# Kernel optimization log

Hardware: AMD Instinct MI355X
Metric: run time of the kernel (lower is better)

Reference implementation:

```python
import jax, jax.numpy as jnp
import numpy as np

B, T, D, H = 2, 2048, 1024, 16
NEG = -65504.0


def setup_inputs() -> dict:
    key = jax.random.key(0)
    ks = jax.random.split(key, 12)
    std = float(np.sqrt(2.0 / (D + D)))  # xavier_normal for square weights
    inp = {
        'q': jax.random.normal(ks[0], (B, T, D), jnp.float32),
        'k': jax.random.normal(ks[1], (B, T, D), jnp.float32),
        'v': jax.random.normal(ks[2], (B, T, D), jnp.float32),
        'mask': jax.random.randint(ks[3], (B, T), 0, 2, jnp.int32),
        # weights stored as (in, out) so y = x @ W + b
        'Wq': jax.random.normal(ks[4], (D, D), jnp.float32) * std,
        'bq': jnp.zeros((D,), jnp.float32),
        'Wk': jax.random.normal(ks[5], (D, D), jnp.float32) * std,
        'bk': jnp.zeros((D,), jnp.float32),
        'Wv': jax.random.normal(ks[6], (D, D), jnp.float32) * std,
        'bv': jnp.zeros((D,), jnp.float32),
        'Wo': jax.random.normal(ks[7], (D, D), jnp.float32) * std,
        'bo': jnp.zeros((D,), jnp.float32),
    }
    return inp


def reference(q, k, v, mask, Wq, bq, Wk, bk, Wv, bv, Wo, bo):
    b, t, _ = q.shape
    dim_a = Wq.shape[1]
    dh = dim_a // H
    # projections, then split into heads: (b, t, H, dh)
    qh = (q @ Wq + bq).reshape(b, t, H, dh)
    kh = (k @ Wk + bk).reshape(b, t, H, dh)
    vh = (v @ Wv + bv).reshape(b, t, H, dh)
    # NOTE: module scales by 1/sqrt(dim_a) with the FULL dim_a, not per-head
    a = jnp.einsum('bthd,bshd->bhts', qh, kh) / jnp.sqrt(jnp.float32(dim_a))
    # 2D mask broadcasts over query positions: (b, 1, 1, t_keys)
    a = jnp.where(mask[:, None, None, :] == 0, NEG, a)
    a = jax.nn.softmax(a, axis=-1)  # dropout_prob=0 (eval mode)
    o = jnp.einsum('bhts,bshd->bthd', a, vh).reshape(b, t, dim_a)
    return o @ Wo + bo
```

## Files before the change

kernel.cpp:

```cpp
#include <hip/hip_runtime.h>
#include <hip/hip_bf16.h>
#include <math.h>

#define B_ 2
#define T_ 2048
#define D_ 1024
#define H_ 16
#define QSCALE (0.03125f * 1.44269504088896f)

typedef _Float16 f16;
using f16x4 = __attribute__((ext_vector_type(4))) _Float16;
using f16x8 = __attribute__((ext_vector_type(8))) _Float16;
using f32x4 = __attribute__((ext_vector_type(4))) float;

__device__ __forceinline__ void gl16(const void* g, void* l) {
  __builtin_amdgcn_global_load_lds(
      (__attribute__((address_space(1))) void*)g,
      (__attribute__((address_space(3))) void*)l, 16, 0, 0);
}

__global__ __launch_bounds__(256) void prep(
    const float* __restrict__ q, const float* __restrict__ k,
    const float* __restrict__ v, const int* __restrict__ mask,
    const float* __restrict__ Wq, const float* __restrict__ Wk,
    const float* __restrict__ Wv, const float* __restrict__ Wo,
    const float* __restrict__ bq, const float* __restrict__ bk,
    const float* __restrict__ bv, const float* __restrict__ bo,
    f16* __restrict__ xqkv, f16* __restrict__ Wt, float* __restrict__ bias,
    int* __restrict__ idx, int* __restrict__ inv, int* __restrict__ nk,
    f16* __restrict__ khc) {
  __shared__ float sh[64][65];
  const int bid = blockIdx.x;
  const int tid = threadIdx.x;

  if (bid < 6144) {
    const int z = bid / 2048;
    const float* src = (z == 0) ? q : (z == 1) ? k : v;
    const size_t i = ((size_t)(bid % 2048) * 256 + tid) * 8;
    float4 a = *(const float4*)(src + i);
    float4 b = *(const float4*)(src + i + 4);
    f16x8 o;
    o[0] = (f16)a.x; o[1] = (f16)a.y; o[2] = (f16)a.z; o[3] = (f16)a.w;
    o[4] = (f16)b.x; o[5] = (f16)b.y; o[6] = (f16)b.z; o[7] = (f16)b.w;
    *(f16x8*)(xqkv + (size_t)z * 4194304 + i) = o;
  } else if (bid < 7168) {
    const int id = bid - 6144;
    const int z = id >> 8;
    const int k0 = ((id >> 4) & 15) * 64, n0 = (id & 15) * 64;
    const float* W = (z == 0) ? Wq : (z == 1) ? Wk : (z == 2) ? Wv : Wo;
    const int r = tid >> 2, c0 = (tid & 3) * 16;
#pragma unroll
    for (int i = 0; i < 4; ++i)
      *(float4*)&sh[r][c0 + 4 * i] =
          *(const float4*)&W[(size_t)(k0 + r) * 1024 + n0 + c0 + 4 * i];
    __syncthreads();
    f16 tmp[16];
#pragma unroll
    for (int i = 0; i < 16; ++i) tmp[i] = (f16)sh[c0 + i][r];
    f16* dst = Wt + (size_t)z * 1048576 + (size_t)(n0 + r) * 1024 + k0 + c0;
    *(f16x8*)dst = *(f16x8*)&tmp[0];
    *(f16x8*)(dst + 8) = *(f16x8*)&tmp[8];
  } else if (bid < 7184) {
    const int i = (bid - 7168) * 256 + tid;
    const int z = i >> 10;
    const float* s = (z == 0) ? bq : (z == 1) ? bk : (z == 2) ? bv : bo;
    bias[i] = s[i & 1023];
  } else {
    const int b = bid - 7184;
    int* cnt = (int*)sh;
    int loc[8];
    int c = 0;
#pragma unroll
    for (int i = 0; i < 8; ++i) {
      loc[i] = mask[b * T_ + tid * 8 + i];
      c += loc[i];
    }
    cnt[tid] = c;
    __syncthreads();
    for (int off = 1; off < 256; off <<= 1) {
      int vsh = (tid >= off) ? cnt[tid - off] : 0;
      __syncthreads();
      cnt[tid] += vsh;
      __syncthreads();
    }
    int pos = cnt[tid] - c;
#pragma unroll
    for (int i = 0; i < 8; ++i) {
      const int t = tid * 8 + i;
      if (loc[i]) {
        idx[b * T_ + pos] = t;
        inv[b * T_ + t] = pos;
        ++pos;
      } else {
        inv[b * T_ + t] = -1;
      }
    }
    const int n = cnt[255];
    if (tid == 255) nk[b] = n;
    const int nkt = (n + 63) >> 6;
    const int npadrows = (nkt << 6) - n;
    uint4 z4 = {0u, 0u, 0u, 0u};
    f16* base = khc + ((size_t)b * T_ + n) * D_;
    for (int i = tid; i < npadrows * 128; i += 256)
      *(uint4*)(base + (size_t)i * 8) = z4;
  }
}

__global__ __launch_bounds__(256) void gemm_qkv(
    const f16* __restrict__ Xb, const f16* __restrict__ Wtb,
    const float* __restrict__ biasb, f16* __restrict__ qh,
    f16* __restrict__ khc, f16* __restrict__ vh,
    const int* __restrict__ inv) {
  __shared__ __align__(16) f16 As[128 * 32];
  __shared__ __align__(16) f16 Bs[128 * 32];
  const int z = blockIdx.z;
  const f16* X = Xb + (size_t)z * 4194304;
  const f16* Wt = Wtb + (size_t)z * 1048576;
  const float* bias = biasb + (size_t)z * 1024;
  f16* C = (z == 0) ? qh : (z == 1) ? khc : vh;

  const int tid = threadIdx.x;
  const int wave = tid >> 6, lane = tid & 63;
  const int quad = lane >> 4, l16 = lane & 15;
  const int wm = wave & 1, wn = wave >> 1;
  const int m0 = blockIdx.y * 128, n0 = blockIdx.x * 128;

  f32x4 acc[4][4] = {};

  const f16* asrc = X + (size_t)(m0 + (tid >> 2)) * 1024 + (tid & 3) * 8;
  const f16* bsrc = Wt + (size_t)(n0 + (tid >> 2)) * 1024 + (tid & 3) * 8;
  char* aldst = (char*)As + tid * 16;
  char* bldst = (char*)Bs + tid * 16;

  for (int kt = 0; kt < 32; ++kt) {
    if (kt) __syncthreads();
    gl16(asrc, aldst);
    gl16(asrc + 65536, aldst + 4096);
    gl16(bsrc, bldst);
    gl16(bsrc + 65536, bldst + 4096);
    asrc += 32; bsrc += 32;
    __syncthreads();

    f16x8 af[4], bf[4];
#pragma unroll
    for (int t = 0; t < 4; ++t)
      af[t] = *(const f16x8*)&As[(64 * wm + 16 * t + l16) * 32 + quad * 8];
#pragma unroll
    for (int t = 0; t < 4; ++t)
      bf[t] = *(const f16x8*)&Bs[(64 * wn + 16 * t + l16) * 32 + quad * 8];
#pragma unroll
    for (int i = 0; i < 4; ++i)
#pragma unroll
      for (int j = 0; j < 4; ++j)
        acc[i][j] = __builtin_amdgcn_mfma_f32_16x16x32_f16(af[i], bf[j], acc[i][j], 0, 0, 0);
  }

  const int cm = m0 + 64 * wm + 4 * quad;
  const int cn = n0 + 64 * wn + l16;
  float bv[4];
#pragma unroll
  for (int tn = 0; tn < 4; ++tn) bv[tn] = bias[cn + 16 * tn];

  if (z == 1) {
    const int bb = m0 >> 11;
#pragma unroll
    for (int tm = 0; tm < 4; ++tm) {
#pragma unroll
      for (int r = 0; r < 4; ++r) {
        const int m = cm + 16 * tm + r;
        const int j = inv[m];
        if (j >= 0) {
          f16* row = C + ((size_t)(bb << 11) + j) * 1024;
#pragma unroll
          for (int tn = 0; tn < 4; ++tn)
            row[cn + 16 * tn] = (f16)(acc[tm][tn][r] + bv[tn]);
        }
      }
    }
  } else {
    const float scl = (z == 0) ? QSCALE : 1.f;
#pragma unroll
    for (int tm = 0; tm < 4; ++tm)
#pragma unroll
      for (int r = 0; r < 4; ++r) {
        f16* row = C + (size_t)(cm + 16 * tm + r) * 1024;
#pragma unroll
        for (int tn = 0; tn < 4; ++tn)
          row[cn + 16 * tn] = (f16)((acc[tm][tn][r] + bv[tn]) * scl);
      }
  }
}

__global__ __launch_bounds__(256) void vtrans(
    const f16* __restrict__ vh, const int* __restrict__ idx,
    const int* __restrict__ nk, f16* __restrict__ vhT) {
  const int tt = blockIdx.x, bh = blockIdx.y;
  const int b = bh >> 4, h = bh & 15;
  const int n = nk[b];
  const int nkt = (n + 63) >> 6;
  if (tt >= nkt) return;
  __shared__ f16 t[64][72];
  const int tid = threadIdx.x;
  const int r = tid >> 2, cq = 16 * (tid & 3);

  const int j = tt * 64 + r;
  uint4 v0 = {0u, 0u, 0u, 0u}, v1 = {0u, 0u, 0u, 0u};
  if (j < n) {
    const int tsrc = idx[b * T_ + j];
    const uint4* src = (const uint4*)(vh + ((size_t)b * T_ + tsrc) * D_ + h * 64 + cq);
    v0 = src[0]; v1 = src[1];
  }
  *(uint4*)&t[r][cq]     = v0;
  *(uint4*)&t[r][cq + 8] = v1;
  __syncthreads();

  f16 tmp[16];
#pragma unroll
  for (int xx = 0; xx < 16; ++xx) {
    int x = (xx + r) & 15;
    tmp[x] = t[cq + x][r];
  }
  f16* dst = vhT + ((size_t)bh * 64 + r) * T_ + tt * 64 + cq;
  *(uint4*)&dst[0] = *(uint4*)&tmp[0];
  *(uint4*)&dst[8] = *(uint4*)&tmp[8];
}

__global__ __launch_bounds__(256) void attn_mfma(
    const f16* __restrict__ qh, const f16* __restrict__ khc,
    const f16* __restrict__ vhT, const int* __restrict__ nkd,
    f16* __restrict__ opart, float* __restrict__ lpart) {
  __shared__ f16 Ks[64][72];
  __shared__ f16 Vt[64][72];
  __shared__ f16 Ps[4][32][72];

  const int qt = blockIdx.x, bh = blockIdx.y, ks = blockIdx.z;
  const int b = bh >> 4, h = bh & 15;
  const int tid = threadIdx.x;
  const int wave = tid >> 6, lane = tid & 63;
  const int quad = lane >> 4, l16 = lane & 15;
  const int sr = tid >> 2, sq = 16 * (tid & 3);

  const int n = nkd[b];
  const int nkt = (n + 63) >> 6;
  const int hn = (nkt + 1) >> 1;
  const int t_begin = ks ? hn : 0;
  const int t_end = ks ? nkt : hn;
  const bool owns_last = (t_end == nkt) && (t_end > t_begin);
  const int npad = (nkt << 6) - n;

  f16x8 qf[2][2];
#pragma unroll
  for (int gq = 0; gq < 2; ++gq) {
    const f16* qp = qh + ((size_t)(b * T_ + qt * 128 + wave * 32 + 16 * gq + l16)) * D_ + h * 64 + quad * 8;
    qf[gq][0] = *(const f16x8*)qp;
    qf[gq][1] = *(const f16x8*)(qp + 32);
  }

  float lsum[2] = {0.f, 0.f};
  f32x4 o[2][4] = {};

  const f16* kbase = khc + (size_t)b * T_ * D_ + h * 64;
  const f16* vbase = vhT + ((size_t)bh * 64 + sr) * T_;

  uint4 kr0, kr1, vr0, vr1;
  auto load_kv = [&](int kt) {
    const uint4* kp = (const uint4*)(kbase + (size_t)(kt * 64 + sr) * D_ + sq);
    kr0 = kp[0]; kr1 = kp[1];
    const uint4* vp = (const uint4*)(vbase + kt * 64 + sq);
    vr0 = vp[0]; vr1 = vp[1];
  };
  if (t_begin < t_end) load_kv(t_begin);

  for (int kt = t_begin; kt < t_end; ++kt) {
    *(uint4*)&Ks[sr][sq]     = kr0;
    *(uint4*)&Ks[sr][sq + 8] = kr1;
    *(uint4*)&Vt[sr][sq]     = vr0;
    *(uint4*)&Vt[sr][sq + 8] = vr1;
    __syncthreads();
    if (kt + 1 < t_end) load_kv(kt + 1);

#pragma unroll
    for (int tn = 0; tn < 4; ++tn) {
      f16x8 kf0 = *(const f16x8*)&Ks[16 * tn + l16][quad * 8];
      f16x8 kf1 = *(const f16x8*)&Ks[16 * tn + l16][32 + quad * 8];
#pragma unroll
      for (int gq = 0; gq < 2; ++gq) {
        f32x4 s = {0.f, 0.f, 0.f, 0.f};
        s = __builtin_amdgcn_mfma_f32_16x16x32_f16(kf0, qf[gq][0], s, 0, 0, 0);
        s = __builtin_amdgcn_mfma_f32_16x16x32_f16(kf1, qf[gq][1], s, 0, 0, 0);
        float p0 = exp2f(s[0]), p1 = exp2f(s[1]);
        float p2 = exp2f(s[2]), p3 = exp2f(s[3]);
        lsum[gq] += (p0 + p1) + (p2 + p3);
        f16x4 pk;
        pk[0] = (f16)p0; pk[1] = (f16)p1; pk[2] = (f16)p2; pk[3] = (f16)p3;
        *(f16x4*)&Ps[wave][16 * gq + l16][16 * tn + 4 * quad] = pk;
      }
    }

    f16x8 pf[2][2];
#pragma unroll
    for (int gq = 0; gq < 2; ++gq) {
      pf[gq][0] = *(const f16x8*)&Ps[wave][16 * gq + l16][quad * 8];
      pf[gq][1] = *(const f16x8*)&Ps[wave][16 * gq + l16][32 + quad * 8];
    }
#pragma unroll
    for (int t = 0; t < 4; ++t) {
      f16x8 vf0 = *(const f16x8*)&Vt[16 * t + l16][quad * 8];
      f16x8 vf1 = *(const f16x8*)&Vt[16 * t + l16][32 + quad * 8];
#pragma unroll
      for (int gq = 0; gq < 2; ++gq) {
        o[gq][t] = __builtin_amdgcn_mfma_f32_16x16x32_f16(pf[gq][0], vf0, o[gq][t], 0, 0, 0);
        o[gq][t] = __builtin_amdgcn_mfma_f32_16x16x32_f16(pf[gq][1], vf1, o[gq][t], 0, 0, 0);
      }
    }
    __syncthreads();
  }

  f16* obase = opart + (size_t)ks * 4194304;
  float* lbase = lpart + (size_t)ks * 65536 + (size_t)bh * 2048;
#pragma unroll
  for (int gq = 0; gq < 2; ++gq) {
    float ls = lsum[gq];
    ls += __shfl_xor(ls, 16);
    ls += __shfl_xor(ls, 32);
    if (owns_last) ls -= (float)npad;
    const int qrow0 = qt * 128 + wave * 32 + 16 * gq;
    if (quad == 0) lbase[qrow0 + l16] = ls;
    const size_t orow = (size_t)(b * T_ + qrow0 + 4 * quad);
#pragma unroll
    for (int r = 0; r < 4; ++r)
#pragma unroll
      for (int t = 0; t < 4; ++t)
        obase[(orow + r) * D_ + h * 64 + 16 * t + l16] = (f16)o[gq][t][r];
  }
}

__global__ __launch_bounds__(256) void gemm_out(
    const f16* __restrict__ opart, const float* __restrict__ lpart,
    const f16* __restrict__ Wt3, const float* __restrict__ bias3,
    float* __restrict__ out) {
  __shared__ __align__(16) f16 As[64 * 32];
  __shared__ __align__(16) f16 Bs[128 * 32];
  const int tid = threadIdx.x;
  const int wave = tid >> 6, lane = tid & 63;
  const int quad = lane >> 4, l16 = lane & 15;
  const int wm = wave & 1, wn = wave >> 1;
  const int m0 = blockIdx.y * 64, n0 = blockIdx.x * 128;

  f32x4 acc[2][4] = {};

  const int row = m0 + (tid >> 2);
  const int cq = (tid & 3) * 8;
  const f16* oa = opart + (size_t)row * 1024 + cq;
  const f16* ob = oa + 4194304;
  const float* lp = lpart + (size_t)(row >> 11) * 32768 + (row & 2047);
  const f16* bsrc = Wt3 + (size_t)(n0 + (tid >> 2)) * 1024 + cq;
  char* bldst = (char*)Bs + tid * 16;

  for (int kt = 0; kt < 32; ++kt) {
    if (kt) __syncthreads();
    gl16(bsrc, bldst);
    gl16(bsrc + 65536, bldst + 4096);
    bsrc += 32;
    const int h = (kt * 32 + cq) >> 6;
    const float la = lp[h * 2048];
    const float lb = lp[65536 + h * 2048];
    const float invl = 1.f / (la + lb);
    f16x8 a8 = *(const f16x8*)(oa + kt * 32);
    f16x8 b8 = *(const f16x8*)(ob + kt * 32);
    f16x8 hv;
#pragma unroll
    for (int i = 0; i < 8; ++i)
      hv[i] = (f16)(((float)a8[i] + (float)b8[i]) * invl);
    *(f16x8*)(As + tid * 8) = hv;
    __syncthreads();

    f16x8 af[2], bf[4];
#pragma unroll
    for (int t = 0; t < 2; ++t)
      af[t] = *(const f16x8*)&As[(32 * wm + 16 * t + l16) * 32 + quad * 8];
#pragma unroll
    for (int t = 0; t < 4; ++t)
      bf[t] = *(const f16x8*)&Bs[(64 * wn + 16 * t + l16) * 32 + quad * 8];
#pragma unroll
    for (int i = 0; i < 2; ++i)
#pragma unroll
      for (int j = 0; j < 4; ++j)
        acc[i][j] = __builtin_amdgcn_mfma_f32_16x16x32_f16(af[i], bf[j], acc[i][j], 0, 0, 0);
  }

  const int cm = m0 + 32 * wm + 4 * quad;
  const int cn = n0 + 64 * wn + l16;
#pragma unroll
  for (int tn = 0; tn < 4; ++tn) {
    const float bv = bias3[cn + 16 * tn];
#pragma unroll
    for (int tm = 0; tm < 2; ++tm)
#pragma unroll
      for (int r = 0; r < 4; ++r)
        out[(size_t)(cm + 16 * tm + r) * 1024 + cn + 16 * tn] = acc[tm][tn][r] + bv;
  }
}

extern "C" void kernel_launch(void* const* d_in, const int* in_sizes, int n_in,
                              void* d_out, int out_size, void* d_ws, size_t ws_size,
                              hipStream_t stream) {
  const float* q  = (const float*)d_in[0];
  const float* k  = (const float*)d_in[1];
  const float* v  = (const float*)d_in[2];
  const int* mask = (const int*)d_in[3];
  const float* Wq = (const float*)d_in[4];
  const float* bq = (const float*)d_in[5];
  const float* Wk = (const float*)d_in[6];
  const float* bk = (const float*)d_in[7];
  const float* Wv = (const float*)d_in[8];
  const float* bv = (const float*)d_in[9];
  const float* Wo = (const float*)d_in[10];
  const float* bo = (const float*)d_in[11];
  float* out = (float*)d_out;

  char* ws = (char*)d_ws;
  f16* xqkv   = (f16*)(ws);
  f16* Wt     = (f16*)(ws + 25165824);
  f16* qh     = (f16*)(ws + 33554432);
  f16* vh     = (f16*)(ws + 41943040);
  f16* khc    = (f16*)(ws + 50331648);
  float* lpart = (float*)(ws + 58720256);
  float* bsw  = (float*)(ws + 59244544);
  int* idx    = (int*)(ws + 59260928);
  int* inv    = (int*)(ws + 59277312);
  int* nk     = (int*)(ws + 59293696);
  f16* vhT    = (f16*)(ws);
  f16* opart  = (f16*)(ws + 8388608);

  dim3 blk(256);

  prep<<<dim3(7186), blk, 0, stream>>>(q, k, v, mask, Wq, Wk, Wv, Wo,
                                       bq, bk, bv, bo, xqkv, Wt, bsw,
                                       idx, inv, nk, khc);

  gemm_qkv<<<dim3(8, 32, 3), blk, 0, stream>>>(xqkv, Wt, bsw,
                                               qh, khc, vh, inv);

  vtrans<<<dim3(32, 32), blk, 0, stream>>>(vh, idx, nk, vhT);

  attn_mfma<<<dim3(16, 32, 2), blk, 0, stream>>>(qh, khc, vhT, nk,
                                                 opart, lpart);

  gemm_out<<<dim3(8, 64), blk, 0, stream>>>(opart, lpart, Wt + 3145728,
                                            bsw + 3072, out);
}
```

Baseline: 230.4 us.

## Remap block IDs for XCD-local L2 reuse and prefetch A operand in out-proj

All three kernels (QKV GEMM, attention, output GEMM) now remap the linear block ID so that blocks sharing the same rows or heads land on the same XCD. The aim is better L2 reuse of shared A tiles and K/V data across the chiplets. In gemm_out, the 16 per-head reciprocal softmax normalisers are computed once up front. The next A-operand partial outputs are also loaded into registers one iteration early, so global latency overlaps the MFMA work. The trade-off is extra register pressure from the invl array and the prefetched vectors.

```diff
diff --git a/kernel.cpp b/kernel.cpp
--- a/kernel.cpp
+++ b/kernel.cpp
@@ -113,7 +113,14 @@
     const int* __restrict__ inv) {
   __shared__ __align__(16) f16 As[128 * 32];
   __shared__ __align__(16) f16 Bs[128 * 32];
-  const int z = blockIdx.z;
+
+  const int bid = blockIdx.x + 8 * blockIdx.y + 256 * blockIdx.z;
+  const int xcd = bid & 7, local = bid >> 3;
+  const int gid = xcd * 12 + (local >> 3);
+  const int z = gid >> 5;
+  const int m0 = (gid & 31) * 128;
+  const int n0 = (local & 7) * 128;
+
   const f16* X = Xb + (size_t)z * 4194304;
   const f16* Wt = Wtb + (size_t)z * 1048576;
   const float* bias = biasb + (size_t)z * 1024;
@@ -123,7 +130,6 @@
   const int wave = tid >> 6, lane = tid & 63;
   const int quad = lane >> 4, l16 = lane & 15;
   const int wm = wave & 1, wn = wave >> 1;
-  const int m0 = blockIdx.y * 128, n0 = blockIdx.x * 128;
 
   f32x4 acc[4][4] = {};
 
@@ -233,8 +239,13 @@
   __shared__ f16 Vt[64][72];
   __shared__ f16 Ps[4][32][72];
 
-  const int qt = blockIdx.x, bh = blockIdx.y, ks = blockIdx.z;
+  const int bid = blockIdx.x + 16 * blockIdx.y + 512 * blockIdx.z;
+  const int xcd = bid & 7, local = bid >> 3;
+  const int qt = local & 15;
+  const int gh = xcd * 8 + (local >> 4);
+  const int bh = gh & 31, ks = gh >> 5;
   const int b = bh >> 4, h = bh & 15;
+
   const int tid = threadIdx.x;
   const int wave = tid >> 6, lane = tid & 63;
   const int quad = lane >> 4, l16 = lane & 15;
@@ -345,7 +356,11 @@
   const int wave = tid >> 6, lane = tid & 63;
   const int quad = lane >> 4, l16 = lane & 15;
   const int wm = wave & 1, wn = wave >> 1;
-  const int m0 = blockIdx.y * 64, n0 = blockIdx.x * 128;
+
+  const int bid = blockIdx.x + 8 * blockIdx.y;
+  const int xcd = bid & 7, local = bid >> 3;
+  const int m0 = (xcd * 8 + (local >> 3)) * 64;
+  const int n0 = (local & 7) * 128;
 
   f32x4 acc[2][4] = {};
 
@@ -354,26 +369,34 @@
   const f16* oa = opart + (size_t)row * 1024 + cq;
   const f16* ob = oa + 4194304;
   const float* lp = lpart + (size_t)(row >> 11) * 32768 + (row & 2047);
+
+  float invl[16];
+#pragma unroll
+  for (int h = 0; h < 16; ++h)
+    invl[h] = 1.f / (lp[h * 2048] + lp[65536 + h * 2048]);
+
   const f16* bsrc = Wt3 + (size_t)(n0 + (tid >> 2)) * 1024 + cq;
   char* bldst = (char*)Bs + tid * 16;
+
+  f16x8 a8 = *(const f16x8*)oa;
+  f16x8 b8 = *(const f16x8*)ob;
 
   for (int kt = 0; kt < 32; ++kt) {
     if (kt) __syncthreads();
     gl16(bsrc, bldst);
     gl16(bsrc + 65536, bldst + 4096);
     bsrc += 32;
-    const int h = (kt * 32 + cq) >> 6;
-    const float la = lp[h * 2048];
-    const float lb = lp[65536 + h * 2048];
-    const float invl = 1.f / (la + lb);
-    f16x8 a8 = *(const f16x8*)(oa + kt * 32);
-    f16x8 b8 = *(const f16x8*)(ob + kt * 32);
+    const float iv = invl[(kt * 32 + cq) >> 6];
     f16x8 hv;
 #pragma unroll
     for (int i = 0; i < 8; ++i)
-      hv[i] = (f16)(((float)a8[i] + (float)b8[i]) * invl);
+      hv[i] = (f16)(((float)a8[i] + (float)b8[i]) * iv);
     *(f16x8*)(As + tid * 8) = hv;
     __syncthreads();
+    if (kt + 1 < 32) {
+      a8 = *(const f16x8*)(oa + (kt + 1) * 32);
+      b8 = *(const f16x8*)(ob + (kt + 1) * 32);
+    }
 
     f16x8 af[2], bf[4];
 #pragma unroll
```

New measurement: 232.5 us. Within noise of the previous version (+0.9%).
